# Kernel tuning notes

Hardware: AMD Instinct MI355X
Metric: run time of the kernel (lower is better)

The kernel has to match this reference:

```python
import jax, jax.numpy as jnp
import numpy as np

D, H, DFF, DC = 1024, 16, 4096, 768
DH = D // H
EPS = 1e-5

def layer_norm(x, g, b):
    m = jnp.mean(x, axis=-1, keepdims=True)
    v = jnp.mean(jnp.square(x - m), axis=-1, keepdims=True)
    return (x - m) * jax.lax.rsqrt(v + EPS) * g + b

def setup_inputs() -> dict:
    key = jax.random.key(0)
    ks = jax.random.split(key, 20)
    s = 0.02
    return {
        "x": jax.random.normal(ks[0], (2, 2048, D), jnp.float32),
        "cond": jax.random.normal(ks[1], (2, 77, DC), jnp.float32),
        # self-attention params
        "Wqkv": jax.random.normal(ks[2], (D, 3 * D), jnp.float32) * s,
        "Wproj_sa": jax.random.normal(ks[3], (D, D), jnp.float32) * s,
        "bproj_sa": jnp.zeros((D,), jnp.float32),
        "g1": jnp.ones((D,), jnp.float32),
        "b1": jnp.zeros((D,), jnp.float32),
        # cross-attention params
        "Wq_ca": jax.random.normal(ks[4], (D, D), jnp.float32) * s,
        "Wkv_ca": jax.random.normal(ks[5], (DC, 2 * D), jnp.float32) * s,
        "Wproj_ca": jax.random.normal(ks[6], (D, D), jnp.float32) * s,
        "bproj_ca": jnp.zeros((D,), jnp.float32),
        "g2": jnp.ones((D,), jnp.float32),
        "b2": jnp.zeros((D,), jnp.float32),
        # feed-forward params
        "Wff1": jax.random.normal(ks[7], (D, DFF), jnp.float32) * s,
        "bff1": jnp.zeros((DFF,), jnp.float32),
        "Wff2": jax.random.normal(ks[8], (DFF, D), jnp.float32) * s,
        "bff2": jnp.zeros((D,), jnp.float32),
        "g3": jnp.ones((D,), jnp.float32),
        "b3": jnp.zeros((D,), jnp.float32),
    }

def _self_attn(x, Wqkv, Wproj, bproj):
    B, T, _ = x.shape
    qkv = x @ Wqkv                                   # (B,T,3D)
    qkv = qkv.reshape(B, T, 3, H, DH)
    q, k, v = (qkv[:, :, i].transpose(0, 2, 1, 3) for i in range(3))  # (B,H,T,DH)
    scale = DH ** -0.5
    attn = jnp.einsum('bhtd,bhsd->bhts', q, k) * scale  # (B,H,T,T)
    causal = jnp.triu(jnp.ones((T, T), bool), k=1)
    attn = jnp.where(causal, -jnp.inf, attn)
    attn = jax.nn.softmax(attn, axis=-1)
    out = jnp.einsum('bhts,bhsd->bhtd', attn, v)
    out = out.transpose(0, 2, 1, 3).reshape(B, T, D)
    return out @ Wproj + bproj

def _cross_attn(x, cond, Wq, Wkv, Wproj, bproj):
    B, T, _ = x.shape
    C = cond.shape[1]
    q = (x @ Wq).reshape(B, T, H, DH).transpose(0, 2, 1, 3)      # (B,H,T,DH)
    kv = (cond @ Wkv).reshape(B, C, 2, H, DH)
    k = kv[:, :, 0].transpose(0, 2, 1, 3)                         # (B,H,C,DH)
    v = kv[:, :, 1].transpose(0, 2, 1, 3)
    scale = DH ** -0.5
    attn = jax.nn.softmax(jnp.einsum('bhtd,bhcd->bhtc', q, k) * scale, axis=-1)
    out = jnp.einsum('bhtc,bhcd->bhtd', attn, v)
    out = out.transpose(0, 2, 1, 3).reshape(B, T, D)
    return out @ Wproj + bproj

def reference(x, cond, Wqkv, Wproj_sa, bproj_sa, g1, b1,
              Wq_ca, Wkv_ca, Wproj_ca, bproj_ca, g2, b2,
              Wff1, bff1, Wff2, bff2, g3, b3):
    x = x + _self_attn(layer_norm(x, g1, b1), Wqkv, Wproj_sa, bproj_sa)
    x = x + _cross_attn(layer_norm(x, g2, b2), cond, Wq_ca, Wkv_ca, Wproj_ca, bproj_ca)
    h = layer_norm(x, g3, b3)
    h = jax.nn.gelu(h @ Wff1 + bff1, approximate=False) @ Wff2 + bff2
    return x + h
```

## Files before the change

### kernel.cpp

```cpp
#include <hip/hip_runtime.h>

using bf16   = __bf16;
using bf16x8 = __attribute__((ext_vector_type(8))) bf16;
using bf16x4 = __attribute__((ext_vector_type(4))) bf16;
using f32x4  = __attribute__((ext_vector_type(4))) float;

#define DEV static __device__ __forceinline__

DEV void MFMA16(bf16x8 a, bf16x8 b, f32x4& c){
  c = __builtin_amdgcn_mfma_f32_16x16x32_bf16(a, b, c, 0, 0, 0);
}

DEV void gload16(const bf16* g, bf16* lds){
  __builtin_amdgcn_global_load_lds(
      (const __attribute__((address_space(1))) void*)g,
      (__attribute__((address_space(3))) void*)lds, 16, 0, 0);
}

DEV void tcast4_dev(const float* __restrict__ in, bf16* __restrict__ out,
                    int R, int C, int bx, int by, float scale, int nscale,
                    int tid, float (*t)[129])
{
  const int c0 = bx*128, r0 = by*32;
  #pragma unroll
  for (int i = 0; i < 4; ++i){
    int row = i*8 + (tid >> 5);
    int col = (tid & 31) * 4;
    const float4 v = *(const float4*)&in[(size_t)(r0+row)*C + c0 + col];
    t[row][col+0]=v.x; t[row][col+1]=v.y; t[row][col+2]=v.z; t[row][col+3]=v.w;
  }
  __syncthreads();
  const int c = tid >> 1, rh = (tid & 1) * 16;
  const float sc = (c0 + c < nscale) ? scale : 1.f;
  bf16 tmp[16];
  #pragma unroll
  for (int j = 0; j < 16; ++j) tmp[j] = (bf16)(t[rh+j][c] * sc);
  bf16* o = out + (size_t)(c0+c)*R + r0 + rh;
  *(bf16x8*)o       = *(bf16x8*)&tmp[0];
  *(bf16x8*)(o + 8) = *(bf16x8*)&tmp[8];
}

DEV void ln_dev(const float* __restrict__ x, const float* __restrict__ gw,
                const float* __restrict__ bw, bf16* __restrict__ y,
                int row, int tid, float (*red)[4])
{
  const float4 v = ((const float4*)(x + (size_t)row*1024))[tid];
  float s  = v.x+v.y+v.z+v.w;
  float s2 = v.x*v.x+v.y*v.y+v.z*v.z+v.w*v.w;
  #pragma unroll
  for (int off=32; off>=1; off>>=1){ s += __shfl_down(s,off); s2 += __shfl_down(s2,off); }
  const int wid = tid>>6, lane = tid&63;
  if (lane==0){ red[0][wid]=s; red[1][wid]=s2; }
  __syncthreads();
  s  = red[0][0]+red[0][1]+red[0][2]+red[0][3];
  s2 = red[1][0]+red[1][1]+red[1][2]+red[1][3];
  const float m  = s*(1.f/1024.f);
  const float rs = rsqrtf(s2*(1.f/1024.f) - m*m + 1e-5f);
  const float4 gv = ((const float4*)gw)[tid];
  const float4 bv = ((const float4*)bw)[tid];
  bf16* yr = y + (size_t)row*1024 + tid*4;
  yr[0] = (bf16)((v.x-m)*rs*gv.x + bv.x);
  yr[1] = (bf16)((v.y-m)*rs*gv.y + bv.y);
  yr[2] = (bf16)((v.z-m)*rs*gv.z + bv.z);
  yr[3] = (bf16)((v.w-m)*rs*gv.w + bv.w);
}

__global__ __launch_bounds__(256) void prep_ln(
    const float* Wqkv, bf16* wqkvT, const float* Wps, bf16* wpsT,
    const float* Wqc, bf16* wqcT, const float* Wkvc, bf16* wkvcT,
    const float* Wpc, bf16* wpcT, const float* Wf1, bf16* wf1T,
    const float* Wf2, bf16* wf2T, const float* cond, bf16* condb,
    const float* x, const float* g1, const float* b1, bf16* xn)
{
  __shared__ float t[32][129];
  __shared__ float red[2][4];
  const int bid = blockIdx.x, tid = threadIdx.x;
  if      (bid <  768) tcast4_dev(Wqkv, wqkvT, 1024, 3072, bid%24,        bid/24,        0.125f, 1024, tid, t);
  else if (bid < 1024) tcast4_dev(Wps,  wpsT,  1024, 1024, (bid-768)%8,   (bid-768)/8,   1.f, 0, tid, t);
  else if (bid < 1280) tcast4_dev(Wqc,  wqcT,  1024, 1024, (bid-1024)%8,  (bid-1024)/8,  0.125f, 1024, tid, t);
  else if (bid < 1664) tcast4_dev(Wkvc, wkvcT,  768, 2048, (bid-1280)%16, (bid-1280)/16, 1.f, 0, tid, t);
  else if (bid < 1920) tcast4_dev(Wpc,  wpcT,  1024, 1024, (bid-1664)%8,  (bid-1664)/8,  1.f, 0, tid, t);
  else if (bid < 2944) tcast4_dev(Wf1,  wf1T,  1024, 4096, (bid-1920)%32, (bid-1920)/32, 1.f, 0, tid, t);
  else if (bid < 3968) tcast4_dev(Wf2,  wf2T,  4096, 1024, (bid-2944)%8,  (bid-2944)/8,  1.f, 0, tid, t);
  else if (bid < 4084) {
    int i = (bid-3968)*256 + tid;
    if (i < 29568) {
      const float4 v = ((const float4*)cond)[i];
      bf16 o[4] = {(bf16)v.x,(bf16)v.y,(bf16)v.z,(bf16)v.w};
      *(bf16x4*)&condb[i*4] = *(bf16x4*)o;
    }
  } else {
    ln_dev(x, g1, b1, xn, bid - 4084, tid, red);
  }
}

__global__ __launch_bounds__(256) void ln_kernel(const float* __restrict__ x,
    const float* __restrict__ gw, const float* __restrict__ bw, bf16* __restrict__ y)
{
  __shared__ float red[2][4];
  ln_dev(x, gw, bw, y, blockIdx.x, threadIdx.x, red);
}

template<int MODE>
__global__ __launch_bounds__(512) void gemm256p(
    const bf16* __restrict__ A, const bf16* __restrict__ Bt,
    const float* __restrict__ bias, const float* resid,
    void* outp, int M, int N, int K)
{
  __shared__ __align__(16) bf16 As[2][256*64];
  __shared__ __align__(16) bf16 Bs[2][256*64];
  const int tid = threadIdx.x;
  const int lane = tid & 63, wid = tid >> 6;
  const int l15 = lane & 15, lh = lane >> 4;
  const int wm = wid >> 2, wn = wid & 3;

  const int nwg = gridDim.x * gridDim.y;
  const int lin = blockIdx.y * gridDim.x + blockIdx.x;
  const int wg  = (lin & 7) * (nwg >> 3) + (lin >> 3);
  const size_t m0 = (size_t)(wg / gridDim.x) * 256;
  const size_t n0 = (size_t)(wg % gridDim.x) * 256;

  f32x4 acc[8][4];
  #pragma unroll
  for (int i=0;i<8;++i)
    #pragma unroll
    for (int j=0;j<4;++j) acc[i][j] = (f32x4){0.f,0.f,0.f,0.f};

  const int srow8 = lane >> 3;
  const int scol  = ((lane & 7) ^ srow8) * 8;
  const int NT = K >> 6;

  auto stageH = [&](int t, int j){
    if (t >= NT) return;
    const int k0 = t << 6;
    const int buf = t & 1;
    const int hl = j & 1;
    const bf16* src = (j < 2) ? A : Bt;
    const size_t base = (j < 2) ? m0 : n0;
    bf16* dst = (j < 2) ? &As[buf][0] : &Bs[buf][0];
    #pragma unroll
    for (int i = 0; i < 2; ++i) {
      int r = hl*128 + wid*16 + i*8;
      gload16(src + (base + (size_t)(r + srow8))*K + k0 + scol, dst + r*64);
    }
  };
  auto rdA = [&](int buf, int mh, int kk, bf16x8* dst){
    #pragma unroll
    for (int i=0;i<4;++i){
      int row = wm*128 + (mh*4+i)*16 + l15;
      dst[i] = *(const bf16x8*)&As[buf][row*64 + (((kk*4+lh) ^ (row&7))<<3)];
    }
  };
  auto rdB = [&](int buf, int kk, bf16x8* dst){
    #pragma unroll
    for (int n=0;n<4;++n){
      int row = wn*64 + n*16 + l15;
      dst[n] = *(const bf16x8*)&Bs[buf][row*64 + (((kk*4+lh) ^ (row&7))<<3)];
    }
  };

  stageH(0,0); stageH(0,1); stageH(0,2); stageH(0,3);
  stageH(1,0); stageH(1,1);
  if (NT > 1) asm volatile("s_waitcnt vmcnt(4)" ::: "memory");
  else        asm volatile("s_waitcnt vmcnt(0)" ::: "memory");
  __builtin_amdgcn_sched_barrier(0);
  __builtin_amdgcn_s_barrier();

  for (int t = 0; t < NT; ++t) {
    const int buf = t & 1;
    bf16x8 af0k0[4], af0k1[4], af1k0[4], af1k1[4], bfr0[4], bfr1[4];
    rdA(buf,0,0,af0k0); rdA(buf,0,1,af0k1); rdB(buf,0,bfr0);
    stageH(t+1,2);
    __builtin_amdgcn_s_barrier();
    asm volatile("s_waitcnt lgkmcnt(0)" ::: "memory");
    __builtin_amdgcn_sched_barrier(0);
    __builtin_amdgcn_s_setprio(1);
    #pragma unroll
    for (int mi=0;mi<4;++mi)
      #pragma unroll
      for (int ni=0;ni<4;++ni) MFMA16(af0k0[mi], bfr0[ni], acc[mi][ni]);
    __builtin_amdgcn_s_setprio(0);
    __builtin_amdgcn_sched_barrier(0);
    __builtin_amdgcn_s_barrier();
    rdA(buf,1,0,af1k0); rdA(buf,1,1,af1k1); rdB(buf,1,bfr1);
    stageH(t+1,3);
    __builtin_amdgcn_s_barrier();
    asm volatile("s_waitcnt lgkmcnt(0)" ::: "memory");
    __builtin_amdgcn_sched_barrier(0);
    __builtin_amdgcn_s_setprio(1);
    #pragma unroll
    for (int mi=0;mi<4;++mi)
      #pragma unroll
      for (int ni=0;ni<4;++ni) MFMA16(af1k0[mi], bfr0[ni], acc[4+mi][ni]);
    __builtin_amdgcn_s_setprio(0);
    __builtin_amdgcn_sched_barrier(0);
    __builtin_amdgcn_s_barrier();
    stageH(t+2,0);
    stageH(t+2,1);
    __builtin_amdgcn_s_setprio(1);
    #pragma unroll
    for (int mi=0;mi<4;++mi)
      #pragma unroll
      for (int ni=0;ni<4;++ni) MFMA16(af0k1[mi], bfr1[ni], acc[mi][ni]);
    #pragma unroll
    for (int mi=0;mi<4;++mi)
      #pragma unroll
      for (int ni=0;ni<4;++ni) MFMA16(af1k1[mi], bfr1[ni], acc[4+mi][ni]);
    __builtin_amdgcn_s_setprio(0);
    if (t + 2 < NT) asm volatile("s_waitcnt vmcnt(4)" ::: "memory");
    else            asm volatile("s_waitcnt vmcnt(0)" ::: "memory");
    __builtin_amdgcn_sched_barrier(0);
    __builtin_amdgcn_s_barrier();
  }

  #pragma unroll
  for (int mi=0;mi<8;++mi){
    #pragma unroll
    for (int r=0;r<4;++r){
      size_t row = m0 + wm*128 + mi*16 + 4*lh + r;
      #pragma unroll
      for (int ni=0;ni<4;++ni){
        size_t col = n0 + wn*64 + ni*16 + l15;
        float v = acc[mi][ni][r];
        if (MODE==0) ((bf16*)outp)[row*(size_t)N + col] = (bf16)v;
        else if (MODE==1) ((float*)outp)[row*(size_t)N + col] = v + bias[col] + resid[row*(size_t)N + col];
        else { v += bias[col];
               ((bf16*)outp)[row*(size_t)N + col] =
                   (bf16)(0.5f*v*(1.0f + erff(v*0.70710678f))); }
      }
    }
  }
}

template<int MODE>
__global__ __launch_bounds__(256) void gemm_bt(
    const bf16* __restrict__ A, const bf16* __restrict__ Bt,
    const float* __restrict__ bias, const float* resid,
    void* outp, int M, int N, int K)
{
  __shared__ __align__(16) bf16 As[2][128*64];
  __shared__ __align__(16) bf16 Bs[2][128*64];
  const int tid = threadIdx.x;
  const int lane = tid & 63, wid = tid >> 6;
  const int l15 = lane & 15, lh = lane >> 4;
  const int wm = wid >> 1, wn = wid & 1;

  const int nwg = gridDim.x * gridDim.y;
  const int lin = blockIdx.y * gridDim.x + blockIdx.x;
  const int wg  = (lin & 7) * (nwg >> 3) + (lin >> 3);
  const size_t m0 = (size_t)(wg / gridDim.x) * 128;
  const size_t n0 = (size_t)(wg % gridDim.x) * 128;

  f32x4 acc[4][4];
  #pragma unroll
  for (int i=0;i<4;++i)
    #pragma unroll
    for (int j=0;j<4;++j) acc[i][j] = (f32x4){0.f,0.f,0.f,0.f};

  const int srow8 = lane >> 3;
  const int scol  = ((lane & 7) ^ srow8) * 8;

  const int NT = K >> 6;

  #pragma unroll
  for (int i = 0; i < 4; ++i) {
    int r = wid*32 + i*8;
    int ar = (int)m0 + r + srow8; if (ar >= M) ar = M - 1;
    gload16(A  + (size_t)ar*K + scol,                 &As[0][r*64]);
    gload16(Bt + (n0 + (size_t)(r + srow8))*K + scol, &Bs[0][r*64]);
  }
  __syncthreads();

  for (int t = 0; t < NT; ++t) {
    const int cur = t & 1;
    if (t + 1 < NT) {
      const int k0 = (t+1) << 6;
      #pragma unroll
      for (int i = 0; i < 4; ++i) {
        int r = wid*32 + i*8;
        int ar = (int)m0 + r + srow8; if (ar >= M) ar = M - 1;
        gload16(A  + (size_t)ar*K + k0 + scol,                 &As[cur^1][r*64]);
        gload16(Bt + (n0 + (size_t)(r + srow8))*K + k0 + scol, &Bs[cur^1][r*64]);
      }
    }
    #pragma unroll
    for (int kk = 0; kk < 2; ++kk) {
      bf16x8 af[4], bfr[4];
      #pragma unroll
      for (int i=0;i<4;++i){
        const int arow = wm*64 + i*16 + l15;
        const int brow = wn*64 + i*16 + l15;
        af[i]  = *(const bf16x8*)&As[cur][arow*64 + (((kk*4+lh) ^ (arow&7))<<3)];
        bfr[i] = *(const bf16x8*)&Bs[cur][brow*64 + (((kk*4+lh) ^ (brow&7))<<3)];
      }
      #pragma unroll
      for (int mi=0;mi<4;++mi)
        #pragma unroll
        for (int ni=0;ni<4;++ni)
          MFMA16(af[mi], bfr[ni], acc[mi][ni]);
    }
    __syncthreads();
  }

  #pragma unroll
  for (int mi=0;mi<4;++mi){
    #pragma unroll
    for (int r=0;r<4;++r){
      size_t row = m0 + wm*64 + mi*16 + 4*lh + r;
      if (row < (size_t)M) {
        #pragma unroll
        for (int ni=0;ni<4;++ni){
          size_t col = n0 + wn*64 + ni*16 + l15;
          float v = acc[mi][ni][r];
          if (MODE==0) ((bf16*)outp)[row*(size_t)N + col] = (bf16)v;
          else if (MODE==1) ((float*)outp)[row*(size_t)N + col] = v + bias[col] + resid[row*(size_t)N + col];
          else { v += bias[col];
                 ((bf16*)outp)[row*(size_t)N + col] =
                     (bf16)(0.5f*v*(1.0f + erff(v*0.70710678f))); }
        }
      }
    }
  }
}

template<int MODE>
__global__ __launch_bounds__(256) void gemm32(
    const bf16* __restrict__ A, const bf16* __restrict__ Bt,
    const float* __restrict__ bias, const float* resid,
    void* outp, int M, int N, int K)
{
  __shared__ __align__(16) bf16 As[2][32*64];
  __shared__ __align__(16) bf16 Bs[2][128*64];
  const int tid = threadIdx.x;
  const int lane = tid & 63, wid = tid >> 6;
  const int l15 = lane & 15, lh = lane >> 4;

  const int nwg = gridDim.x * gridDim.y;
  const int lin = blockIdx.y * gridDim.x + blockIdx.x;
  const int wg  = (lin & 7) * (nwg >> 3) + (lin >> 3);
  const size_t m0 = (size_t)(wg / gridDim.x) * 32;
  const size_t n0 = (size_t)(wg % gridDim.x) * 128;

  f32x4 acc[2][2];
  #pragma unroll
  for (int i=0;i<2;++i)
    #pragma unroll
    for (int j=0;j<2;++j) acc[i][j] = (f32x4){0.f,0.f,0.f,0.f};

  const int srow8 = lane >> 3;
  const int scol  = ((lane & 7) ^ srow8) * 8;

  const int NT = K >> 6;

  {
    int r = wid*8;
    gload16(A + (m0 + (size_t)(r + srow8))*K + scol, &As[0][r*64]);
  }
  #pragma unroll
  for (int i = 0; i < 4; ++i) {
    int r = wid*32 + i*8;
    gload16(Bt + (n0 + (size_t)(r + srow8))*K + scol, &Bs[0][r*64]);
  }
  __syncthreads();

  for (int t = 0; t < NT; ++t) {
    const int cur = t & 1;
    if (t + 1 < NT) {
      const int k0 = (t+1) << 6;
      {
        int r = wid*8;
        gload16(A + (m0 + (size_t)(r + srow8))*K + k0 + scol, &As[cur^1][r*64]);
      }
      #pragma unroll
      for (int i = 0; i < 4; ++i) {
        int r = wid*32 + i*8;
        gload16(Bt + (n0 + (size_t)(r + srow8))*K + k0 + scol, &Bs[cur^1][r*64]);
      }
    }
    #pragma unroll
    for (int kk = 0; kk < 2; ++kk) {
      bf16x8 af[2], bfr[2];
      #pragma unroll
      for (int i=0;i<2;++i){
        const int arow = i*16 + l15;
        af[i]  = *(const bf16x8*)&As[cur][arow*64 + (((kk*4+lh) ^ (arow&7))<<3)];
      }
      #pragma unroll
      for (int n=0;n<2;++n){
        const int brow = wid*32 + n*16 + l15;
        bfr[n] = *(const bf16x8*)&Bs[cur][brow*64 + (((kk*4+lh) ^ (brow&7))<<3)];
      }
      #pragma unroll
      for (int mi=0;mi<2;++mi)
        #pragma unroll
        for (int ni=0;ni<2;++ni)
          MFMA16(af[mi], bfr[ni], acc[mi][ni]);
    }
    __syncthreads();
  }

  #pragma unroll
  for (int mi=0;mi<2;++mi){
    #pragma unroll
    for (int r=0;r<4;++r){
      size_t row = m0 + mi*16 + 4*lh + r;
      #pragma unroll
      for (int ni=0;ni<2;++ni){
        size_t col = n0 + wid*32 + ni*16 + l15;
        float v = acc[mi][ni][r];
        if (MODE==0) ((bf16*)outp)[row*(size_t)N + col] = (bf16)v;
        else if (MODE==1) ((float*)outp)[row*(size_t)N + col] = v + bias[col] + resid[row*(size_t)N + col];
        else { v += bias[col];
               ((bf16*)outp)[row*(size_t)N + col] =
                   (bf16)(0.5f*v*(1.0f + erff(v*0.70710678f))); }
      }
    }
  }
}

__global__ __launch_bounds__(256) void vtsa_kernel(const bf16* __restrict__ qkv, bf16* __restrict__ vt)
{
  __shared__ bf16 t[32][33];
  const int b = blockIdx.z >> 4, h = blockIdx.z & 15;
  const int s0 = blockIdx.x*32, d0 = blockIdx.y*32;
  const int tx = threadIdx.x & 31, ty = threadIdx.x >> 5;
  #pragma unroll
  for (int i = ty; i < 32; i += 8)
    t[i][tx] = qkv[(size_t)(b*2048 + s0+i)*3072 + 2048 + h*64 + d0 + tx];
  __syncthreads();
  #pragma unroll
  for (int i = ty; i < 32; i += 8)
    vt[((size_t)blockIdx.z*64 + d0+i)*2048 + s0 + tx] = t[tx][i];
}

__global__ __launch_bounds__(256) void kvca_re(const bf16* __restrict__ kvca,
    bf16* __restrict__ kpad, bf16* __restrict__ vtca)
{
  int idx = blockIdx.x*256 + threadIdx.x;
  if (idx >= 2*16*128*64) return;
  int d = idx & 63, s = (idx>>6) & 127, h = (idx>>13) & 15, b = idx>>17;
  bf16 kv = (bf16)0.f, vv = (bf16)0.f;
  if (s < 77) {
    kv = kvca[(size_t)(b*77+s)*2048 + h*64 + d];
    vv = kvca[(size_t)(b*77+s)*2048 + 1024 + h*64 + d];
  }
  kpad[idx] = kv;
  vtca[(((size_t)(b*16+h)*64 + d)<<7) + s] = vv;
}

template<int CAUSAL>
__global__ __launch_bounds__(256) void flash6(
    const bf16* __restrict__ qb, long q_bstride, long qstride,
    const bf16* __restrict__ kb0, long k_bstride, long k_hstride, long kstride,
    const bf16* __restrict__ vtb, long vt_bhstride, long vtstride,
    bf16* __restrict__ out, int skv)
{
  __shared__ __align__(16) bf16 Ks[2][64*64];
  __shared__ __align__(16) bf16 Vs[2][64*64];
  __shared__ __align__(16) bf16 Ps[4][16*68];
  const int tid = threadIdx.x;
  const int w = tid >> 6, lane = tid & 63, l15 = lane & 15, lh = lane >> 4;
  const int bid = blockIdx.x;
  const int bh   = (bid & 7) + 8*((bid >> 3) & 3);
  const int tile = 31 - (bid >> 5);
  const int b = bh >> 4, h = bh & 15;
  const int q0 = tile * 64;
  const int nkb   = CAUSAL ? tile + 1 : ((skv + 63) >> 6);
  const int nfull = CAUSAL ? tile     : (skv >> 6);

  const bf16* kbase = kb0 + (size_t)b*k_bstride + (size_t)h*k_hstride;
  const bf16* vbase = vtb + (size_t)bh*vt_bhstride;
  const int sr0 = tid >> 3, sslot = tid & 7;

  const bf16* qrow = qb + (size_t)b*q_bstride + (size_t)h*64
                        + (size_t)(q0 + w*16 + l15)*qstride;
  bf16x8 qf0 = *(const bf16x8*)(qrow + 8*lh);
  bf16x8 qf1 = *(const bf16x8*)(qrow + 32 + 8*lh);

  f32x4 o[4];
  #pragma unroll
  for (int i=0;i<4;++i) o[i] = (f32x4){0.f,0.f,0.f,0.f};
  float lacc[4] = {0.f,0.f,0.f,0.f};

  bf16x8 kreg[2], vreg[2];
  #pragma unroll
  for (int i=0;i<2;++i){
    int r = sr0 + 32*i;
    kreg[i] = *(const bf16x8*)(kbase + (size_t)r*kstride + sslot*8);
    vreg[i] = *(const bf16x8*)(vbase + (size_t)r*vtstride + sslot*8);
  }

  for (int kb = 0; kb < nkb; ++kb) {
    const int buf = kb & 1;
    #pragma unroll
    for (int i=0;i<2;++i){
      int r = sr0 + 32*i;
      int ps = (sslot ^ (r & 7)) * 8;
      *(bf16x8*)&Ks[buf][r*64 + ps] = kreg[i];
      *(bf16x8*)&Vs[buf][r*64 + ps] = vreg[i];
    }
    __syncthreads();
    if (kb + 1 < nkb) {
      #pragma unroll
      for (int i=0;i<2;++i){
        int r = sr0 + 32*i;
        kreg[i] = *(const bf16x8*)(kbase + (size_t)((kb+1)*64 + r)*kstride + sslot*8);
        vreg[i] = *(const bf16x8*)(vbase + (size_t)r*vtstride + (kb+1)*64 + sslot*8);
      }
    }
    f32x4 sf[4];
    __builtin_amdgcn_s_setprio(1);
    #pragma unroll
    for (int ni = 0; ni < 4; ++ni) {
      int kr = ni*16 + l15;
      bf16x8 kf0 = *(const bf16x8*)&Ks[buf][kr*64 + (((lh  ) ^ (kr&7))<<3)];
      bf16x8 kf1 = *(const bf16x8*)&Ks[buf][kr*64 + (((lh+4) ^ (kr&7))<<3)];
      f32x4 z = (f32x4){0.f,0.f,0.f,0.f};
      MFMA16(qf0, kf0, z);
      MFMA16(qf1, kf1, z);
      sf[ni] = z;
    }
    __builtin_amdgcn_s_setprio(0);
    if (kb >= nfull) {
      #pragma unroll
      for (int ni=0;ni<4;++ni){
        int col = kb*64 + ni*16 + l15;
        #pragma unroll
        for (int r=0;r<4;++r){
          int rowg = q0 + w*16 + 4*lh + r;
          if (col >= skv || (CAUSAL && col > rowg)) sf[ni][r] = -1e30f;
        }
      }
    }
    #pragma unroll
    for (int ni=0;ni<4;++ni){
      #pragma unroll
      for (int r=0;r<4;++r){
        float p = __expf(sf[ni][r]);
        lacc[r] += p;
        Ps[w][(4*lh + r)*68 + ni*16 + l15] = (bf16)p;
      }
    }
    bf16x8 pa0 = *(const bf16x8*)&Ps[w][l15*68 + 8*lh];
    bf16x8 pa1 = *(const bf16x8*)&Ps[w][l15*68 + 32 + 8*lh];
    __builtin_amdgcn_s_setprio(1);
    #pragma unroll
    for (int nd=0;nd<4;++nd){
      int vr = nd*16 + l15;
      bf16x8 vf0 = *(const bf16x8*)&Vs[buf][vr*64 + (((lh  ) ^ (vr&7))<<3)];
      bf16x8 vf1 = *(const bf16x8*)&Vs[buf][vr*64 + (((lh+4) ^ (vr&7))<<3)];
      MFMA16(pa0, vf0, o[nd]);
      MFMA16(pa1, vf1, o[nd]);
    }
    __builtin_amdgcn_s_setprio(0);
  }
  float lr[4];
  #pragma unroll
  for (int r=0;r<4;++r) lr[r] = lacc[r];
  #pragma unroll
  for (int off=1; off<16; off<<=1)
    #pragma unroll
    for (int r=0;r<4;++r) lr[r] += __shfl_xor(lr[r], off);
  #pragma unroll
  for (int nd=0;nd<4;++nd)
    #pragma unroll
    for (int r=0;r<4;++r){
      int rowg = q0 + w*16 + 4*lh + r;
      out[(size_t)(b*2048 + rowg)*1024 + h*64 + nd*16 + l15] =
          (bf16)(o[nd][r] / lr[r]);
    }
}

struct Bump { char* base; size_t off;
  void* get(size_t bytes){ void* p = base + off; off += (bytes + 255) & ~(size_t)255; return p; } };

extern "C" void kernel_launch(void* const* d_in, const int* in_sizes, int n_in,
                              void* d_out, int out_size, void* d_ws, size_t ws_size,
                              hipStream_t stream)
{
  const float* x        = (const float*)d_in[0];
  const float* cond     = (const float*)d_in[1];
  const float* Wqkv     = (const float*)d_in[2];
  const float* Wproj_sa = (const float*)d_in[3];
  const float* bproj_sa = (const float*)d_in[4];
  const float* g1       = (const float*)d_in[5];
  const float* b1       = (const float*)d_in[6];
  const float* Wq_ca    = (const float*)d_in[7];
  const float* Wkv_ca   = (const float*)d_in[8];
  const float* Wproj_ca = (const float*)d_in[9];
  const float* bproj_ca = (const float*)d_in[10];
  const float* g2       = (const float*)d_in[11];
  const float* b2       = (const float*)d_in[12];
  const float* Wff1     = (const float*)d_in[13];
  const float* bff1     = (const float*)d_in[14];
  const float* Wff2     = (const float*)d_in[15];
  const float* bff2     = (const float*)d_in[16];
  const float* g3       = (const float*)d_in[17];
  const float* b3       = (const float*)d_in[18];

  Bump bump{(char*)d_ws, 0};
  bf16* wqkvT    = (bf16*)bump.get((size_t)3072*1024*2);
  bf16* wprojSaT = (bf16*)bump.get((size_t)1024*1024*2);
  bf16* wqCaT    = (bf16*)bump.get((size_t)1024*1024*2);
  bf16* wkvCaT   = (bf16*)bump.get((size_t)2048*768*2);
  bf16* wprojCaT = (bf16*)bump.get((size_t)1024*1024*2);
  bf16* wff1T    = (bf16*)bump.get((size_t)4096*1024*2);
  bf16* wff2T    = (bf16*)bump.get((size_t)1024*4096*2);
  bf16* condb    = (bf16*)bump.get((size_t)154*768*2);
  bf16* xn       = (bf16*)bump.get((size_t)4096*1024*2);
  bf16* qkv      = (bf16*)bump.get((size_t)4096*3072*2);
  bf16* vt_sa    = (bf16*)bump.get((size_t)2*16*64*2048*2);
  bf16* attn     = (bf16*)bump.get((size_t)4096*1024*2);
  bf16* kvca     = (bf16*)bump.get((size_t)154*2048*2);
  bf16* kpad     = (bf16*)bump.get((size_t)2*16*128*64*2);
  bf16* vtca     = (bf16*)bump.get((size_t)2*16*64*128*2);
  bf16* h1   = qkv;
  bf16* qca  = vt_sa;
  float* x1  = (float*)d_out;

  prep_ln<<<dim3(8180), 256, 0, stream>>>(
      Wqkv, wqkvT, Wproj_sa, wprojSaT, Wq_ca, wqCaT, Wkv_ca, wkvCaT,
      Wproj_ca, wprojCaT, Wff1, wff1T, Wff2, wff2T, cond, condb,
      x, g1, b1, xn);

  gemm256p<0><<<dim3(12,16), 512, 0, stream>>>(xn, wqkvT, nullptr, nullptr, qkv, 4096, 3072, 1024);
  vtsa_kernel<<<dim3(64,2,32), 256, 0, stream>>>(qkv, vt_sa);
  flash6<1><<<dim3(1024), 256, 0, stream>>>(
      qkv,        (long)2048*3072, 3072,
      qkv + 1024, (long)2048*3072, 64, 3072,
      vt_sa,      (long)64*2048, 2048,
      attn, 2048);
  gemm32<1><<<dim3(8,128), 256, 0, stream>>>(attn, wprojSaT, bproj_sa, x, x1, 4096, 1024, 1024);

  ln_kernel<<<dim3(4096), 256, 0, stream>>>(x1, g2, b2, xn);
  gemm32<0><<<dim3(8,128), 256, 0, stream>>>(xn, wqCaT, nullptr, nullptr, qca, 4096, 1024, 1024);
  gemm_bt<0><<<dim3(16,2), 256, 0, stream>>>(condb, wkvCaT, nullptr, nullptr, kvca, 154, 2048, 768);
  kvca_re<<<dim3(1024), 256, 0, stream>>>(kvca, kpad, vtca);
  flash6<0><<<dim3(1024), 256, 0, stream>>>(
      qca,  (long)2048*1024, 1024,
      kpad, (long)16*128*64, (long)128*64, 64,
      vtca, (long)64*128, 128,
      attn, 77);
  gemm32<1><<<dim3(8,128), 256, 0, stream>>>(attn, wprojCaT, bproj_ca, x1, x1, 4096, 1024, 1024);

  ln_kernel<<<dim3(4096), 256, 0, stream>>>(x1, g3, b3, xn);
  gemm256p<2><<<dim3(16,16), 512, 0, stream>>>(xn, wff1T, bff1, nullptr, h1, 4096, 4096, 1024);
  gemm32<1><<<dim3(8,128), 256, 0, stream>>>(h1, wff2T, bff2, x1, d_out, 4096, 1024, 4096);

  (void)in_sizes; (void)n_in; (void)out_size; (void)ws_size;
}
```

Measured before the change: 302.3 us.

## Fold cross-attn KV GEMM and reshape into self-attention-stage kernels

```diff
diff --git a/kernel.cpp b/kernel.cpp
--- a/kernel.cpp
+++ b/kernel.cpp
@@ -232,24 +232,36 @@
   }
 }
 
-template<int MODE>
-__global__ __launch_bounds__(256) void gemm_bt(
-    const bf16* __restrict__ A, const bf16* __restrict__ Bt,
-    const float* __restrict__ bias, const float* resid,
-    void* outp, int M, int N, int K)
-{
+__global__ __launch_bounds__(256) void vtsa_kv(
+    const bf16* __restrict__ qkv, bf16* __restrict__ vt,
+    const bf16* __restrict__ condb, const bf16* __restrict__ wkvCaT,
+    bf16* __restrict__ kvca)
+{
+  __shared__ bf16 t[32][33];
   __shared__ __align__(16) bf16 As[2][128*64];
   __shared__ __align__(16) bf16 Bs[2][128*64];
-  const int tid = threadIdx.x;
+  const int bid = blockIdx.x, tid = threadIdx.x;
+  if (bid < 4096) {
+    const int bx = bid & 63, byy = (bid >> 6) & 1, bz = bid >> 7;
+    const int b = bz >> 4, h = bz & 15;
+    const int s0 = bx*32, d0 = byy*32;
+    const int tx = tid & 31, ty = tid >> 5;
+    #pragma unroll
+    for (int i = ty; i < 32; i += 8)
+      t[i][tx] = qkv[(size_t)(b*2048 + s0+i)*3072 + 2048 + h*64 + d0 + tx];
+    __syncthreads();
+    #pragma unroll
+    for (int i = ty; i < 32; i += 8)
+      vt[((size_t)bz*64 + d0+i)*2048 + s0 + tx] = t[tx][i];
+    return;
+  }
+  const int g = bid - 4096;
+  const int M = 154, N = 2048, K = 768;
   const int lane = tid & 63, wid = tid >> 6;
   const int l15 = lane & 15, lh = lane >> 4;
   const int wm = wid >> 1, wn = wid & 1;
-
-  const int nwg = gridDim.x * gridDim.y;
-  const int lin = blockIdx.y * gridDim.x + blockIdx.x;
-  const int wg  = (lin & 7) * (nwg >> 3) + (lin >> 3);
-  const size_t m0 = (size_t)(wg / gridDim.x) * 128;
-  const size_t n0 = (size_t)(wg % gridDim.x) * 128;
+  const size_t m0 = (size_t)(g >> 4) * 128;
+  const size_t n0 = (size_t)(g & 15) * 128;
 
   f32x4 acc[4][4];
   #pragma unroll
@@ -259,28 +271,27 @@
 
   const int srow8 = lane >> 3;
   const int scol  = ((lane & 7) ^ srow8) * 8;
-
   const int NT = K >> 6;
 
   #pragma unroll
   for (int i = 0; i < 4; ++i) {
     int r = wid*32 + i*8;
     int ar = (int)m0 + r + srow8; if (ar >= M) ar = M - 1;
-    gload16(A  + (size_t)ar*K + scol,                 &As[0][r*64]);
-    gload16(Bt + (n0 + (size_t)(r + srow8))*K + scol, &Bs[0][r*64]);
+    gload16(condb  + (size_t)ar*K + scol,                 &As[0][r*64]);
+    gload16(wkvCaT + (n0 + (size_t)(r + srow8))*K + scol, &Bs[0][r*64]);
   }
   __syncthreads();
 
-  for (int t = 0; t < NT; ++t) {
-    const int cur = t & 1;
-    if (t + 1 < NT) {
-      const int k0 = (t+1) << 6;
+  for (int tt = 0; tt < NT; ++tt) {
+    const int cur = tt & 1;
+    if (tt + 1 < NT) {
+      const int k0 = (tt+1) << 6;
       #pragma unroll
       for (int i = 0; i < 4; ++i) {
         int r = wid*32 + i*8;
         int ar = (int)m0 + r + srow8; if (ar >= M) ar = M - 1;
-        gload16(A  + (size_t)ar*K + k0 + scol,                 &As[cur^1][r*64]);
-        gload16(Bt + (n0 + (size_t)(r + srow8))*K + k0 + scol, &Bs[cur^1][r*64]);
+        gload16(condb  + (size_t)ar*K + k0 + scol,                 &As[cur^1][r*64]);
+        gload16(wkvCaT + (n0 + (size_t)(r + srow8))*K + k0 + scol, &Bs[cur^1][r*64]);
       }
     }
     #pragma unroll
@@ -311,12 +322,7 @@
         #pragma unroll
         for (int ni=0;ni<4;++ni){
           size_t col = n0 + wn*64 + ni*16 + l15;
-          float v = acc[mi][ni][r];
-          if (MODE==0) ((bf16*)outp)[row*(size_t)N + col] = (bf16)v;
-          else if (MODE==1) ((float*)outp)[row*(size_t)N + col] = v + bias[col] + resid[row*(size_t)N + col];
-          else { v += bias[col];
-                 ((bf16*)outp)[row*(size_t)N + col] =
-                     (bf16)(0.5f*v*(1.0f + erff(v*0.70710678f))); }
+          kvca[row*(size_t)N + col] = (bf16)acc[mi][ni][r];
         }
       }
     }
@@ -418,38 +424,8 @@
   }
 }
 
-__global__ __launch_bounds__(256) void vtsa_kernel(const bf16* __restrict__ qkv, bf16* __restrict__ vt)
-{
-  __shared__ bf16 t[32][33];
-  const int b = blockIdx.z >> 4, h = blockIdx.z & 15;
-  const int s0 = blockIdx.x*32, d0 = blockIdx.y*32;
-  const int tx = threadIdx.x & 31, ty = threadIdx.x >> 5;
-  #pragma unroll
-  for (int i = ty; i < 32; i += 8)
-    t[i][tx] = qkv[(size_t)(b*2048 + s0+i)*3072 + 2048 + h*64 + d0 + tx];
-  __syncthreads();
-  #pragma unroll
-  for (int i = ty; i < 32; i += 8)
-    vt[((size_t)blockIdx.z*64 + d0+i)*2048 + s0 + tx] = t[tx][i];
-}
-
-__global__ __launch_bounds__(256) void kvca_re(const bf16* __restrict__ kvca,
-    bf16* __restrict__ kpad, bf16* __restrict__ vtca)
-{
-  int idx = blockIdx.x*256 + threadIdx.x;
-  if (idx >= 2*16*128*64) return;
-  int d = idx & 63, s = (idx>>6) & 127, h = (idx>>13) & 15, b = idx>>17;
-  bf16 kv = (bf16)0.f, vv = (bf16)0.f;
-  if (s < 77) {
-    kv = kvca[(size_t)(b*77+s)*2048 + h*64 + d];
-    vv = kvca[(size_t)(b*77+s)*2048 + 1024 + h*64 + d];
-  }
-  kpad[idx] = kv;
-  vtca[(((size_t)(b*16+h)*64 + d)<<7) + s] = vv;
-}
-
 template<int CAUSAL>
-__global__ __launch_bounds__(256) void flash6(
+DEV void flash6_dev(int bid, int tid,
     const bf16* __restrict__ qb, long q_bstride, long qstride,
     const bf16* __restrict__ kb0, long k_bstride, long k_hstride, long kstride,
     const bf16* __restrict__ vtb, long vt_bhstride, long vtstride,
@@ -458,9 +434,7 @@
   __shared__ __align__(16) bf16 Ks[2][64*64];
   __shared__ __align__(16) bf16 Vs[2][64*64];
   __shared__ __align__(16) bf16 Ps[4][16*68];
-  const int tid = threadIdx.x;
   const int w = tid >> 6, lane = tid & 63, l15 = lane & 15, lh = lane >> 4;
-  const int bid = blockIdx.x;
   const int bh   = (bid & 7) + 8*((bid >> 3) & 3);
   const int tile = 31 - (bid >> 5);
   const int b = bh >> 4, h = bh & 15;
@@ -569,6 +543,42 @@
       out[(size_t)(b*2048 + rowg)*1024 + h*64 + nd*16 + l15] =
           (bf16)(o[nd][r] / lr[r]);
     }
+}
+
+__global__ __launch_bounds__(256) void flash6sa(
+    const bf16* __restrict__ qb, long q_bstride, long qstride,
+    const bf16* __restrict__ kb0, long k_bstride, long k_hstride, long kstride,
+    const bf16* __restrict__ vtb, long vt_bhstride, long vtstride,
+    bf16* __restrict__ out, int skv,
+    const bf16* __restrict__ kvca, bf16* __restrict__ kpad, bf16* __restrict__ vtca)
+{
+  if (blockIdx.x >= 1024) {
+    int idx = (blockIdx.x - 1024)*256 + threadIdx.x;
+    int d = idx & 63, s = (idx>>6) & 127, h = (idx>>13) & 15, b = idx>>17;
+    bf16 kv = (bf16)0.f, vv = (bf16)0.f;
+    if (s < 77) {
+      kv = kvca[(size_t)(b*77+s)*2048 + h*64 + d];
+      vv = kvca[(size_t)(b*77+s)*2048 + 1024 + h*64 + d];
+    }
+    kpad[idx] = kv;
+    vtca[(((size_t)(b*16+h)*64 + d)<<7) + s] = vv;
+    return;
+  }
+  flash6_dev<1>(blockIdx.x, threadIdx.x, qb, q_bstride, qstride,
+                kb0, k_bstride, k_hstride, kstride,
+                vtb, vt_bhstride, vtstride, out, skv);
+}
+
+template<int CAUSAL>
+__global__ __launch_bounds__(256) void flash6(
+    const bf16* __restrict__ qb, long q_bstride, long qstride,
+    const bf16* __restrict__ kb0, long k_bstride, long k_hstride, long kstride,
+    const bf16* __restrict__ vtb, long vt_bhstride, long vtstride,
+    bf16* __restrict__ out, int skv)
+{
+  flash6_dev<CAUSAL>(blockIdx.x, threadIdx.x, qb, q_bstride, qstride,
+                     kb0, k_bstride, k_hstride, kstride,
+                     vtb, vt_bhstride, vtstride, out, skv);
 }
 
 struct Bump { char* base; size_t off;
@@ -624,18 +634,17 @@
       x, g1, b1, xn);
 
   gemm256p<0><<<dim3(12,16), 512, 0, stream>>>(xn, wqkvT, nullptr, nullptr, qkv, 4096, 3072, 1024);
-  vtsa_kernel<<<dim3(64,2,32), 256, 0, stream>>>(qkv, vt_sa);
-  flash6<1><<<dim3(1024), 256, 0, stream>>>(
+  vtsa_kv<<<dim3(4128), 256, 0, stream>>>(qkv, vt_sa, condb, wkvCaT, kvca);
+  flash6sa<<<dim3(2048), 256, 0, stream>>>(
       qkv,        (long)2048*3072, 3072,
       qkv + 1024, (long)2048*3072, 64, 3072,
       vt_sa,      (long)64*2048, 2048,
-      attn, 2048);
+      attn, 2048,
+      kvca, kpad, vtca);
   gemm32<1><<<dim3(8,128), 256, 0, stream>>>(attn, wprojSaT, bproj_sa, x, x1, 4096, 1024, 1024);
 
   ln_kernel<<<dim3(4096), 256, 0, stream>>>(x1, g2, b2, xn);
   gemm32<0><<<dim3(8,128), 256, 0, stream>>>(xn, wqCaT, nullptr, nullptr, qca, 4096, 1024, 1024);
-  gemm_bt<0><<<dim3(16,2), 256, 0, stream>>>(condb, wkvCaT, nullptr, nullptr, kvca, 154, 2048, 768);
-  kvca_re<<<dim3(1024), 256, 0, stream>>>(kvca, kpad, vtca);
   flash6<0><<<dim3(1024), 256, 0, stream>>>(
       qca,  (long)2048*1024, 1024,
       kpad, (long)16*128*64, (long)128*64, 64,
```

Result: no change. 308.0 us (+1.9%).
